# Kernel tuning notes

Hardware: AMD Instinct MI355X
Metric: run time of the kernel (lower is better)

The kernel has to match this reference:

```python
import jax, jax.numpy as jnp
import numpy as np

B, S, D = 2, 2048, 1024
H, DC = 16, 16          # num_heads, head_coord_dim
CD = 16                 # coord_dim
DH = D // H             # head_dim = 64


def setup_inputs() -> dict:
    key = jax.random.key(0)
    ks = jax.random.split(key, 8)
    s = 0.02
    return {
        "hidden_states": jax.random.normal(ks[0], (B, S, D), jnp.float32),
        "coordinates": jax.random.normal(ks[1], (B, S, CD), jnp.float32),
        "Wv": jax.random.normal(ks[2], (D, D), jnp.float32) * s,
        "bv": jnp.zeros((D,), jnp.float32),
        "Wc": jax.random.normal(ks[3], (H * DC, CD), jnp.float32) * s,
        "bc": jnp.zeros((H * DC,), jnp.float32),
        "Wn": jax.random.normal(ks[4], (CD, D), jnp.float32) * s,
        "bn": jnp.zeros((CD,), jnp.float32),
        "Wo": jax.random.normal(ks[5], (D, D), jnp.float32) * s,
        "bo": jnp.zeros((D,), jnp.float32),
        "gamma": jnp.zeros((1, H, 1, 1), jnp.float32),
    }


def reference(hidden_states, coordinates, Wv, bv, Wc, bc, Wn, bn, Wo, bo, gamma):
    # value: [B,S,D] -> [B,H,S,DH]
    value = (hidden_states @ Wv.T + bv).reshape(B, S, H, DH).transpose(0, 2, 1, 3)
    # coordinate heads: [B,S,CD] -> [B,H,S,DC]
    z = (coordinates @ Wc.T + bc).reshape(B, S, H, DC).transpose(0, 2, 1, 3)
    z_sq = jnp.sum(z * z, axis=-1, keepdims=True)           # [B,H,S,1]
    # pairwise squared distances [B,H,S,S]
    sq_dist = z_sq + jnp.swapaxes(z_sq, -1, -2) - 2.0 * jnp.einsum("bhsc,bhtc->bhst", z, z)
    sq_dist = jnp.maximum(sq_dist, 0.0)
    g = jax.nn.softplus(gamma)                               # [1,H,1,1]
    attn = jax.nn.softmax(-g * sq_dist, axis=-1)             # [B,H,S,S]
    out = jnp.einsum("bhst,bhtd->bhsd", attn, value)         # [B,H,S,DH]
    out = out.transpose(0, 2, 1, 3).reshape(B, S, D)
    updated_hidden = out @ Wo.T + bo
    updated_coords = hidden_states @ Wn.T + bn               # [B,S,CD]
    return updated_hidden, updated_coords
```

## Files before the change

kernel.cpp:

```cpp
#include <hip/hip_runtime.h>
#include <math.h>

typedef short short8 __attribute__((ext_vector_type(8)));
typedef short short4t __attribute__((ext_vector_type(4)));
typedef float f32x4  __attribute__((ext_vector_type(4)));

#define AS1 __attribute__((address_space(1)))
#define AS3 __attribute__((address_space(3)))

__device__ __forceinline__ unsigned cvt_pk_bf16(float lo, float hi) {
    unsigned r;
    asm("v_cvt_pk_bf16_f32 %0, %1, %2" : "=v"(r) : "v"(lo), "v"(hi));
    return r;
}
__device__ __forceinline__ unsigned f2bf_rne(float x) {
    unsigned u = __float_as_uint(x);
    return (u + 0x7fffu + ((u >> 16) & 1u)) >> 16;
}
__device__ __forceinline__ float exp2_fast(float x) {
    float r;
    asm("v_exp_f32 %0, %1" : "=v"(r) : "v"(x));
    return r;
}
__device__ __forceinline__ f32x4 mfma_k16(short4t a, short4t b, f32x4 c) {
#if __has_builtin(__builtin_amdgcn_mfma_f32_16x16x16bf16_1k)
    return __builtin_amdgcn_mfma_f32_16x16x16bf16_1k(a, b, c, 0, 0, 0);
#else
    asm volatile("v_mfma_f32_16x16x16_bf16 %0, %1, %2, %0" : "+v"(c) : "v"(a), "v"(b));
    return c;
#endif
}

__global__ __launch_bounds__(256) void f2bf_all(const float* __restrict__ hidden,
                                                const float* __restrict__ Wv,
                                                const float* __restrict__ Wo,
                                                const float* __restrict__ Wn,
                                                short* __restrict__ hsb,
                                                short* __restrict__ Wvb,
                                                short* __restrict__ Wob,
                                                short* __restrict__ Wnb) {
    const int i = blockIdx.x * 256 + threadIdx.x;
    const float* src;
    short* dst;
    int ii;
    if (i < 524288)      { src = hidden; dst = hsb; ii = i; }
    else if (i < 655360) { src = Wv; dst = Wvb; ii = i - 524288; }
    else if (i < 786432) { src = Wo; dst = Wob; ii = i - 655360; }
    else                 { src = Wn; dst = Wnb; ii = i - 786432; }
    const float4 a = ((const float4*)src)[2 * ii];
    const float4 b = ((const float4*)src)[2 * ii + 1];
    uint4 r;
    r.x = cvt_pk_bf16(a.x, a.y);
    r.y = cvt_pk_bf16(a.z, a.w);
    r.z = cvt_pk_bf16(b.x, b.y);
    r.w = cvt_pk_bf16(b.z, b.w);
    ((uint4*)dst)[ii] = r;
}

__global__ __launch_bounds__(256) void zker3(const float* __restrict__ coords,
                                             const float* __restrict__ Wc,
                                             const float* __restrict__ bc,
                                             const float* __restrict__ gamma,
                                             short* __restrict__ ZA,
                                             short* __restrict__ ZB) {
    const int bs = blockIdx.x;
    const int b = bs >> 11, s = bs & 2047;
    const int tid = threadIdx.x;
    __shared__ float csh[16];
    if (tid < 16) csh[tid] = coords[(size_t)bs * 16 + tid];
    __syncthreads();
    float z = bc[tid];
#pragma unroll
    for (int k = 0; k < 16; k++) z = fmaf(csh[k], Wc[tid * 16 + k], z);
    const unsigned ub = f2bf_rne(z);
    const float zb = __uint_as_float(ub << 16);
    float sq = zb * zb;
    sq += __shfl_xor(sq, 1, 64);
    sq += __shfl_xor(sq, 2, 64);
    sq += __shfl_xor(sq, 4, 64);
    sq += __shfl_xor(sq, 8, 64);
    const int h = tid >> 4, c = tid & 15;
    const float gm = gamma[h];
    const float sp = fmaxf(gm, 0.f) + log1pf(__expf(-fabsf(gm)));
    const float ch = -sp * 1.4426950408889634f;
    const size_t row = ((size_t)(b * 16 + h) * 2048 + s) * 32;
    ZA[row + c] = (short)ub;
    ZA[row + 16 + c] = (c == 0) ? (short)f2bf_rne(sq)
                                : (c == 1 ? (short)0x3F80 : (short)0);
    ZB[row + c] = (short)f2bf_rne(-2.f * ch * zb);
    ZB[row + 16 + c] = (c == 0) ? (short)f2bf_rne(ch)
                                : (c == 1 ? (short)f2bf_rne(ch * sq) : (short)0);
}

template <int EPI>
__global__ __launch_bounds__(256) void gemm_mfma(const short* __restrict__ A,
                                                 const short* __restrict__ W,
                                                 const float* __restrict__ bias,
                                                 void* __restrict__ Cout) {
    __shared__ short As[2][128][64];
    __shared__ short Bs[2][64][64];
    const int tid = threadIdx.x;
    const int wv = tid >> 6, l = tid & 63, g = l >> 4, qc = l & 15;
    const int wm = wv >> 1, wn = wv & 1;
    const int Mb = blockIdx.y * 128, Nb = blockIdx.x * 64;

    auto stage = [&](int buf, int k0) {
#pragma unroll
        for (int i = 0; i < 4; i++) {
            const int c = i * 256 + tid;
            const int r = c >> 3, jp = c & 7;
            const int js = jp ^ (r & 7);
            const short* gsA = A + (size_t)(Mb + r) * 1024 + k0 + js * 8;
            short* ldsA = &As[buf][0][0] + (size_t)(i * 256 + wv * 64) * 8;
            __builtin_amdgcn_global_load_lds((const AS1 void*)gsA, (AS3 void*)ldsA, 16, 0, 0);
        }
#pragma unroll
        for (int i = 0; i < 2; i++) {
            const int c = i * 256 + tid;
            const int r = c >> 3, jp = c & 7;
            const int js = jp ^ (r & 7);
            const short* gsB = W + (size_t)(Nb + r) * 1024 + k0 + js * 8;
            short* ldsB = &Bs[buf][0][0] + (size_t)(i * 256 + wv * 64) * 8;
            __builtin_amdgcn_global_load_lds((const AS1 void*)gsB, (AS3 void*)ldsB, 16, 0, 0);
        }
    };

    f32x4 acc[4][2] = {};
    stage(0, 0);
    __syncthreads();
    int cur = 0;
#pragma unroll 1
    for (int kb = 0; kb < 16; kb++) {
        if (kb < 15) stage(cur ^ 1, (kb + 1) * 64);
#pragma unroll
        for (int ks = 0; ks < 2; ks++) {
            const int cs = ((ks * 4 + g) ^ (qc & 7)) * 8;
            short8 af[4], bfr[2];
#pragma unroll
            for (int mt = 0; mt < 4; mt++)
                af[mt] = *(const short8*)&As[cur][wm * 64 + mt * 16 + qc][cs];
#pragma unroll
            for (int nt = 0; nt < 2; nt++)
                bfr[nt] = *(const short8*)&Bs[cur][wn * 32 + nt * 16 + qc][cs];
#pragma unroll
            for (int mt = 0; mt < 4; mt++)
#pragma unroll
                for (int nt = 0; nt < 2; nt++)
                    acc[mt][nt] = __builtin_amdgcn_mfma_f32_16x16x32_bf16(af[mt], bfr[nt], acc[mt][nt], 0, 0, 0);
        }
        __syncthreads();
        cur ^= 1;
    }

    float bl[2];
#pragma unroll
    for (int nt = 0; nt < 2; nt++) bl[nt] = bias[Nb + wn * 32 + nt * 16 + qc];
#pragma unroll
    for (int mt = 0; mt < 4; mt++) {
#pragma unroll
        for (int nt = 0; nt < 2; nt++) {
            const int m0 = Mb + wm * 64 + mt * 16 + g * 4;
            const int n  = Nb + wn * 32 + nt * 16 + qc;
            f32x4 v = acc[mt][nt];
            v = v + bl[nt];
            if (EPI == 0) {
                const int bb = m0 >> 11, s0 = m0 & 2047;
                const int hh = n >> 6, dh = n & 63;
                const int s0x = s0 ^ (((n >> 3) & 1) << 2);
                uint2 p2;
                p2.x = cvt_pk_bf16(v[0], v[1]);
                p2.y = cvt_pk_bf16(v[2], v[3]);
                *(uint2*)((short*)Cout + (size_t)((bb * 16 + hh) * 64 + dh) * 2048 + s0x) = p2;
            } else {
                float* C = (float*)Cout;
#pragma unroll
                for (int i = 0; i < 4; i++) C[(size_t)(m0 + i) * 1024 + n] = v[i];
            }
        }
    }
}

__global__ __launch_bounds__(256, 4) void attn_mfma10(const short* __restrict__ ZAg,
                                                      const short* __restrict__ ZBg,
                                                      const short* __restrict__ Vt,
                                                      short* __restrict__ AOb) {
    __shared__ short Vs[2][4096];
    __shared__ short Zs[3][2048];
    const int tid = threadIdx.x;
    const int wv = tid >> 6, ln = tid & 63, g = ln >> 4, qc = ln & 15;
    const int lin = blockIdx.x;
    const int work = (lin & 7) * 128 + (lin >> 3);
    const int qb = work & 31, h = (work >> 5) & 15, b = work >> 9;
    const int bh = b * 16 + h;
    const int q0 = qb * 64 + wv * 16;

    const short* ZAb = ZAg + (size_t)bh * (2048 * 32);
    const short* ZBb = ZBg + (size_t)bh * (2048 * 32);
    const short* Vb  = Vt  + (size_t)bh * (64 * 2048);

    const short8 zq = *(const short8*)(ZBb + (size_t)(q0 + qc) * 32 + g * 8);

    f32x4 acc[4] = {};
    float lsum = 0.f;

    const short* gvb = Vb + (size_t)ln * 2048 + wv * 8;
    short* lvd = &Vs[0][0] + (size_t)tid * 8;
    short* lzd = &Zs[0][0] + (size_t)tid * 8;
    const int z_kt = tid >> 6, z_g = (tid >> 4) & 3, z_r = tid & 15;

    auto stageV = [&](int buf, int kb) {
        const short* gv = gvb + kb;
        short* lvb = lvd + buf * 4096;
        __builtin_amdgcn_global_load_lds((const AS1 void*)gv, (AS3 void*)lvb, 16, 0, 0);
        __builtin_amdgcn_global_load_lds((const AS1 void*)(gv + 32), (AS3 void*)(lvb + 2048), 16, 0, 0);
    };
    auto stageZ = [&](int buf, int kb) {
        const short* gz = ZAb + (size_t)(kb + z_kt * 16 + z_r) * 32 + z_g * 8;
        __builtin_amdgcn_global_load_lds((const AS1 void*)gz, (AS3 void*)(lzd + buf * 2048), 16, 0, 0);
    };

    const int vrd = (((g >> 1) * 64 + qc) * 8) + (((g & 1) ^ ((qc >> 3) & 1)) << 2);
    const int zrd = g * 128 + qc * 8;

    auto computeP = [&](int zbuf, unsigned pko[4][2], bool doL) {
        const short* Zc = &Zs[0][0] + zbuf * 2048;
        short8 zk[4];
#pragma unroll
        for (int kt = 0; kt < 4; kt++)
            zk[kt] = *(const short8*)(Zc + zrd + kt * 512);
        const f32x4 z4 = {0.f, 0.f, 0.f, 0.f};
#pragma unroll
        for (int kt = 0; kt < 4; kt++) {
            const f32x4 S = __builtin_amdgcn_mfma_f32_16x16x32_bf16(zk[kt], zq, z4, 0, 0, 0);
            const float p0 = exp2_fast(fminf(S[0], 0.f));
            const float p1 = exp2_fast(fminf(S[1], 0.f));
            const float p2 = exp2_fast(fminf(S[2], 0.f));
            const float p3 = exp2_fast(fminf(S[3], 0.f));
            if (doL) lsum += (p0 + p1) + (p2 + p3);
            pko[kt][0] = cvt_pk_bf16(p0, p1);
            pko[kt][1] = cvt_pk_bf16(p2, p3);
        }
    };

    stageV(0, 0);
    stageZ(0, 0);
    stageZ(1, 64);
    __syncthreads();

    unsigned pk[4][2];
    computeP(0, pk, true);

    int cur = 0;
    int zn = 1;
#pragma unroll 1
    for (int i = 0; i < 32; i++) {
        const int kb = i * 64;
        int zs = zn + 1; if (zs == 3) zs = 0;
        if (i < 31) stageV(cur ^ 1, kb + 64);
        if (i < 30) stageZ(zs, kb + 128);

        unsigned pknext[4][2];
        computeP(zn, pknext, i < 31);

        const short* Vc = &Vs[cur][0];
        __builtin_amdgcn_s_setprio(1);
#pragma unroll
        for (int kt = 0; kt < 4; kt++) {
            union { unsigned u[2]; short4t s4; } pb;
            pb.u[0] = pk[kt][0];
            pb.u[1] = pk[kt][1];
#pragma unroll
            for (int mt = 0; mt < 4; mt++)
                acc[mt] = mfma_k16(*(const short4t*)(Vc + vrd + kt * 1024 + mt * 128),
                                   pb.s4, acc[mt]);
        }
        __builtin_amdgcn_s_setprio(0);

#pragma unroll
        for (int kt = 0; kt < 4; kt++) {
            pk[kt][0] = pknext[kt][0];
            pk[kt][1] = pknext[kt][1];
        }

        __syncthreads();
        cur ^= 1;
        zn = zs;
    }

    lsum += __shfl_xor(lsum, 16, 64);
    lsum += __shfl_xor(lsum, 32, 64);
    const float inv = 1.f / lsum;
    const size_t row = (size_t)(b * 2048 + q0 + qc) * 1024 + h * 64;
#pragma unroll
    for (int mt = 0; mt < 4; mt++) {
        uint2 o;
        o.x = cvt_pk_bf16(acc[mt][0] * inv, acc[mt][1] * inv);
        o.y = cvt_pk_bf16(acc[mt][2] * inv, acc[mt][3] * inv);
        *(uint2*)(AOb + row + mt * 16 + g * 4) = o;
    }
}

__global__ __launch_bounds__(256) void coords_mfma(const short* __restrict__ A,
                                                   const short* __restrict__ Wnb,
                                                   const float* __restrict__ bn,
                                                   float* __restrict__ out1) {
    __shared__ float red[4][16][16];
    const int tid = threadIdx.x;
    const int wv = tid >> 6, l = tid & 63, g = l >> 4, qc = l & 15;
    const int m0 = blockIdx.x * 16;
    const int k0 = wv * 256;
    f32x4 acc = {};
#pragma unroll
    for (int kk = 0; kk < 256; kk += 32) {
        const short8 af = *(const short8*)(A + (size_t)(m0 + qc) * 1024 + k0 + kk + g * 8);
        const short8 bf = *(const short8*)(Wnb + (size_t)qc * 1024 + k0 + kk + g * 8);
        acc = __builtin_amdgcn_mfma_f32_16x16x32_bf16(af, bf, acc, 0, 0, 0);
    }
#pragma unroll
    for (int i2 = 0; i2 < 4; i2++) red[wv][g * 4 + i2][qc] = acc[i2];
    __syncthreads();
    const int r = tid >> 4, c = tid & 15;
    const float s = red[0][r][c] + red[1][r][c] + red[2][r][c] + red[3][r][c] + bn[c];
    out1[(size_t)(m0 + r) * 16 + c] = s;
}

extern "C" void kernel_launch(void* const* d_in, const int* in_sizes, int n_in,
                              void* d_out, int out_size, void* d_ws, size_t ws_size,
                              hipStream_t stream) {
    (void)in_sizes; (void)n_in; (void)out_size; (void)ws_size;
    const float* hidden = (const float*)d_in[0];
    const float* coords = (const float*)d_in[1];
    const float* Wv = (const float*)d_in[2];
    const float* bv = (const float*)d_in[3];
    const float* Wc = (const float*)d_in[4];
    const float* bc = (const float*)d_in[5];
    const float* Wn = (const float*)d_in[6];
    const float* bn = (const float*)d_in[7];
    const float* Wo = (const float*)d_in[8];
    const float* bo = (const float*)d_in[9];
    const float* gamma = (const float*)d_in[10];

    char* wsb = (char*)d_ws;
    short* hsb = (short*)(wsb);
    short* AOb = hsb;
    short* Wvb = (short*)(wsb + (8 << 20));
    short* Wob = (short*)(wsb + (10 << 20));
    short* Vt  = (short*)(wsb + (12 << 20));
    short* ZA  = (short*)(wsb + (20 << 20));
    short* ZB  = (short*)(wsb + (24 << 20));
    short* Wnb = (short*)(wsb + (28 << 20));

    float* out_hidden = (float*)d_out;
    float* out_coords = out_hidden + 4194304;

    f2bf_all<<<3080, 256, 0, stream>>>(hidden, Wv, Wo, Wn, hsb, Wvb, Wob, Wnb);
    zker3<<<4096, 256, 0, stream>>>(coords, Wc, bc, gamma, ZA, ZB);
    gemm_mfma<0><<<dim3(16, 32), 256, 0, stream>>>(hsb, Wvb, bv, (void*)Vt);
    coords_mfma<<<256, 256, 0, stream>>>(hsb, Wnb, bn, out_coords);
    attn_mfma10<<<1024, 256, 0, stream>>>(ZA, ZB, Vt, AOb);
    gemm_mfma<1><<<dim3(16, 32), 256, 0, stream>>>(AOb, Wob, bo, (void*)out_hidden);
}
```

Measured before the change: 108.7 us.

## Drop LDS staging in attention; read V and Z directly into registers

The V projection epilogue now writes values in a fragment-friendly tiled layout (16 keys by 64 dims per chunk), so the attention kernel can load MFMA operands straight from global memory into registers. The LDS double/triple buffers and per-iteration __syncthreads are removed. Z keys are prefetched one iteration ahead in registers. The goal is to cut LDS traffic and barrier stalls, at the cost of losing cross-wave sharing of V tiles: each of the four waves now reads the same V chunk from L2/cache separately, and there is less latency hiding.

```diff
diff --git a/kernel.cpp b/kernel.cpp
--- a/kernel.cpp
+++ b/kernel.cpp
@@ -166,11 +166,11 @@
             if (EPI == 0) {
                 const int bb = m0 >> 11, s0 = m0 & 2047;
                 const int hh = n >> 6, dh = n & 63;
-                const int s0x = s0 ^ (((n >> 3) & 1) << 2);
+                const int kc = s0 >> 4, si = s0 & 15;
                 uint2 p2;
                 p2.x = cvt_pk_bf16(v[0], v[1]);
                 p2.y = cvt_pk_bf16(v[2], v[3]);
-                *(uint2*)((short*)Cout + (size_t)((bb * 16 + hh) * 64 + dh) * 2048 + s0x) = p2;
+                *(uint2*)((short*)Cout + (size_t)(bb * 16 + hh) * 131072 + kc * 1024 + dh * 16 + si) = p2;
             } else {
                 float* C = (float*)Cout;
 #pragma unroll
@@ -180,12 +180,10 @@
     }
 }
 
-__global__ __launch_bounds__(256, 4) void attn_mfma10(const short* __restrict__ ZAg,
+__global__ __launch_bounds__(256, 4) void attn_mfma11(const short* __restrict__ ZAg,
                                                       const short* __restrict__ ZBg,
                                                       const short* __restrict__ Vt,
                                                       short* __restrict__ AOb) {
-    __shared__ short Vs[2][4096];
-    __shared__ short Zs[3][2048];
     const int tid = threadIdx.x;
     const int wv = tid >> 6, ln = tid & 63, g = ln >> 4, qc = ln & 15;
     const int lin = blockIdx.x;
@@ -196,73 +194,60 @@
 
     const short* ZAb = ZAg + (size_t)bh * (2048 * 32);
     const short* ZBb = ZBg + (size_t)bh * (2048 * 32);
-    const short* Vb  = Vt  + (size_t)bh * (64 * 2048);
+    const short* Vb  = Vt  + (size_t)bh * 131072;
 
     const short8 zq = *(const short8*)(ZBb + (size_t)(q0 + qc) * 32 + g * 8);
 
     f32x4 acc[4] = {};
     float lsum = 0.f;
 
-    const short* gvb = Vb + (size_t)ln * 2048 + wv * 8;
-    short* lvd = &Vs[0][0] + (size_t)tid * 8;
-    short* lzd = &Zs[0][0] + (size_t)tid * 8;
-    const int z_kt = tid >> 6, z_g = (tid >> 4) & 3, z_r = tid & 15;
-
-    auto stageV = [&](int buf, int kb) {
-        const short* gv = gvb + kb;
-        short* lvb = lvd + buf * 4096;
-        __builtin_amdgcn_global_load_lds((const AS1 void*)gv, (AS3 void*)lvb, 16, 0, 0);
-        __builtin_amdgcn_global_load_lds((const AS1 void*)(gv + 32), (AS3 void*)(lvb + 2048), 16, 0, 0);
-    };
-    auto stageZ = [&](int buf, int kb) {
-        const short* gz = ZAb + (size_t)(kb + z_kt * 16 + z_r) * 32 + z_g * 8;
-        __builtin_amdgcn_global_load_lds((const AS1 void*)gz, (AS3 void*)(lzd + buf * 2048), 16, 0, 0);
-    };
-
-    const int vrd = (((g >> 1) * 64 + qc) * 8) + (((g & 1) ^ ((qc >> 3) & 1)) << 2);
-    const int zrd = g * 128 + qc * 8;
-
-    auto computeP = [&](int zbuf, unsigned pko[4][2], bool doL) {
-        const short* Zc = &Zs[0][0] + zbuf * 2048;
-        short8 zk[4];
-#pragma unroll
-        for (int kt = 0; kt < 4; kt++)
-            zk[kt] = *(const short8*)(Zc + zrd + kt * 512);
-        const f32x4 z4 = {0.f, 0.f, 0.f, 0.f};
-#pragma unroll
-        for (int kt = 0; kt < 4; kt++) {
-            const f32x4 S = __builtin_amdgcn_mfma_f32_16x16x32_bf16(zk[kt], zq, z4, 0, 0, 0);
-            const float p0 = exp2_fast(fminf(S[0], 0.f));
-            const float p1 = exp2_fast(fminf(S[1], 0.f));
-            const float p2 = exp2_fast(fminf(S[2], 0.f));
-            const float p3 = exp2_fast(fminf(S[3], 0.f));
-            if (doL) lsum += (p0 + p1) + (p2 + p3);
-            pko[kt][0] = cvt_pk_bf16(p0, p1);
-            pko[kt][1] = cvt_pk_bf16(p2, p3);
-        }
-    };
-
-    stageV(0, 0);
-    stageZ(0, 0);
-    stageZ(1, 64);
-    __syncthreads();
-
-    unsigned pk[4][2];
-    computeP(0, pk, true);
-
-    int cur = 0;
-    int zn = 1;
+    const short* zbase = ZAb + (size_t)qc * 32 + g * 8;
+    const short* vbase = Vb + qc * 16 + g * 4;
+
+    short8 zkc[4];
+#pragma unroll
+    for (int kt = 0; kt < 4; kt++)
+        zkc[kt] = *(const short8*)(zbase + (size_t)(kt * 16) * 32);
+
 #pragma unroll 1
     for (int i = 0; i < 32; i++) {
         const int kb = i * 64;
-        int zs = zn + 1; if (zs == 3) zs = 0;
-        if (i < 31) stageV(cur ^ 1, kb + 64);
-        if (i < 30) stageZ(zs, kb + 128);
-
-        unsigned pknext[4][2];
-        computeP(zn, pknext, i < 31);
-
-        const short* Vc = &Vs[cur][0];
+
+        short8 zkn[4];
+        if (i < 31) {
+#pragma unroll
+            for (int kt = 0; kt < 4; kt++)
+                zkn[kt] = *(const short8*)(zbase + (size_t)(kb + 64 + kt * 16) * 32);
+        }
+
+        short4t vf[4][4];
+        const short* vk = vbase + (size_t)(i * 4) * 1024;
+#pragma unroll
+        for (int kt = 0; kt < 4; kt++)
+#pragma unroll
+            for (int mt = 0; mt < 4; mt++)
+                vf[kt][mt] = *(const short4t*)(vk + kt * 1024 + mt * 256);
+
+        const f32x4 z4 = {0.f, 0.f, 0.f, 0.f};
+        f32x4 S[4];
+        __builtin_amdgcn_s_setprio(1);
+#pragma unroll
+        for (int kt = 0; kt < 4; kt++)
+            S[kt] = __builtin_amdgcn_mfma_f32_16x16x32_bf16(zkc[kt], zq, z4, 0, 0, 0);
+        __builtin_amdgcn_s_setprio(0);
+
+        unsigned pk[4][2];
+#pragma unroll
+        for (int kt = 0; kt < 4; kt++) {
+            const float p0 = exp2_fast(fminf(S[kt][0], 0.f));
+            const float p1 = exp2_fast(fminf(S[kt][1], 0.f));
+            const float p2 = exp2_fast(fminf(S[kt][2], 0.f));
+            const float p3 = exp2_fast(fminf(S[kt][3], 0.f));
+            lsum += (p0 + p1) + (p2 + p3);
+            pk[kt][0] = cvt_pk_bf16(p0, p1);
+            pk[kt][1] = cvt_pk_bf16(p2, p3);
+        }
+
         __builtin_amdgcn_s_setprio(1);
 #pragma unroll
         for (int kt = 0; kt < 4; kt++) {
@@ -271,20 +256,14 @@
             pb.u[1] = pk[kt][1];
 #pragma unroll
             for (int mt = 0; mt < 4; mt++)
-                acc[mt] = mfma_k16(*(const short4t*)(Vc + vrd + kt * 1024 + mt * 128),
-                                   pb.s4, acc[mt]);
+                acc[mt] = mfma_k16(vf[kt][mt], pb.s4, acc[mt]);
         }
         __builtin_amdgcn_s_setprio(0);
 
-#pragma unroll
-        for (int kt = 0; kt < 4; kt++) {
-            pk[kt][0] = pknext[kt][0];
-            pk[kt][1] = pknext[kt][1];
-        }
-
-        __syncthreads();
-        cur ^= 1;
-        zn = zs;
+        if (i < 31) {
+#pragma unroll
+            for (int kt = 0; kt < 4; kt++) zkc[kt] = zkn[kt];
+        }
     }
 
     lsum += __shfl_xor(lsum, 16, 64);
@@ -357,6 +336,6 @@
     zker3<<<4096, 256, 0, stream>>>(coords, Wc, bc, gamma, ZA, ZB);
     gemm_mfma<0><<<dim3(16, 32), 256, 0, stream>>>(hsb, Wvb, bv, (void*)Vt);
     coords_mfma<<<256, 256, 0, stream>>>(hsb, Wnb, bn, out_coords);
-    attn_mfma10<<<1024, 256, 0, stream>>>(ZA, ZB, Vt, AOb);
+    attn_mfma11<<<1024, 256, 0, stream>>>(ZA, ZB, Vt, AOb);
     gemm_mfma<1><<<dim3(16, 32), 256, 0, stream>>>(AOb, Wob, bo, (void*)out_hidden);
 }
```

After: 147.8 us. 35.9% more time.

## Compute softmax row sums via MFMA, unroll attention loop by two, remap GEMM blocks

Applied to the files above, without the earlier changes.

The attention kernel drops the per-element scalar row-sum accumulation and instead gets the softmax denominator from an extra MFMA against a ones vector. It also unrolls the main loop by two with ping-pong P registers and a four-deep Z buffer, which removes the register copy and the modular buffer arithmetic. The GEMM launches switch to a 1D grid remapped so that consecutive blocks land on different XCDs with grouped M tiles, aiming for better L2 reuse. The trade-offs are more LDS for Z, one extra MFMA per k-tile, and a row sum taken from bf16-rounded P values.

```diff
diff --git a/kernel.cpp b/kernel.cpp
--- a/kernel.cpp
+++ b/kernel.cpp
@@ -102,7 +102,9 @@
     const int tid = threadIdx.x;
     const int wv = tid >> 6, l = tid & 63, g = l >> 4, qc = l & 15;
     const int wm = wv >> 1, wn = wv & 1;
-    const int Mb = blockIdx.y * 128, Nb = blockIdx.x * 64;
+    const int lin = blockIdx.x;
+    const int wid = (lin & 7) * 64 + (lin >> 3);
+    const int Mb = (wid & 31) * 128, Nb = (wid >> 5) * 64;
 
     auto stage = [&](int buf, int k0) {
 #pragma unroll
@@ -180,12 +182,12 @@
     }
 }
 
-__global__ __launch_bounds__(256, 4) void attn_mfma10(const short* __restrict__ ZAg,
+__global__ __launch_bounds__(256, 4) void attn_mfma12(const short* __restrict__ ZAg,
                                                       const short* __restrict__ ZBg,
                                                       const short* __restrict__ Vt,
                                                       short* __restrict__ AOb) {
     __shared__ short Vs[2][4096];
-    __shared__ short Zs[3][2048];
+    __shared__ short Zs[4][2048];
     const int tid = threadIdx.x;
     const int wv = tid >> 6, ln = tid & 63, g = ln >> 4, qc = ln & 15;
     const int lin = blockIdx.x;
@@ -200,8 +202,11 @@
 
     const short8 zq = *(const short8*)(ZBb + (size_t)(q0 + qc) * 32 + g * 8);
 
+    union { unsigned u[2]; short4t s4; } ones4;
+    ones4.u[0] = ones4.u[1] = (qc == 0) ? 0x3F803F80u : 0u;
+
     f32x4 acc[4] = {};
-    float lsum = 0.f;
+    f32x4 accl = {};
 
     const short* gvb = Vb + (size_t)ln * 2048 + wv * 8;
     short* lvd = &Vs[0][0] + (size_t)tid * 8;
@@ -222,7 +227,7 @@
     const int vrd = (((g >> 1) * 64 + qc) * 8) + (((g & 1) ^ ((qc >> 3) & 1)) << 2);
     const int zrd = g * 128 + qc * 8;
 
-    auto computeP = [&](int zbuf, unsigned pko[4][2], bool doL) {
+    auto computeP = [&](int zbuf, unsigned pko[4][2]) {
         const short* Zc = &Zs[0][0] + zbuf * 2048;
         short8 zk[4];
 #pragma unroll
@@ -232,14 +237,25 @@
 #pragma unroll
         for (int kt = 0; kt < 4; kt++) {
             const f32x4 S = __builtin_amdgcn_mfma_f32_16x16x32_bf16(zk[kt], zq, z4, 0, 0, 0);
-            const float p0 = exp2_fast(fminf(S[0], 0.f));
-            const float p1 = exp2_fast(fminf(S[1], 0.f));
-            const float p2 = exp2_fast(fminf(S[2], 0.f));
-            const float p3 = exp2_fast(fminf(S[3], 0.f));
-            if (doL) lsum += (p0 + p1) + (p2 + p3);
-            pko[kt][0] = cvt_pk_bf16(p0, p1);
-            pko[kt][1] = cvt_pk_bf16(p2, p3);
-        }
+            pko[kt][0] = cvt_pk_bf16(exp2_fast(fminf(S[0], 0.f)), exp2_fast(fminf(S[1], 0.f)));
+            pko[kt][1] = cvt_pk_bf16(exp2_fast(fminf(S[2], 0.f)), exp2_fast(fminf(S[3], 0.f)));
+        }
+    };
+    auto doPV = [&](int buf, unsigned pkk[4][2]) {
+        const short* Vc = &Vs[buf][0];
+        __builtin_amdgcn_s_setprio(1);
+#pragma unroll
+        for (int kt = 0; kt < 4; kt++) {
+            union { unsigned u[2]; short4t s4; } pb;
+            pb.u[0] = pkk[kt][0];
+            pb.u[1] = pkk[kt][1];
+            accl = mfma_k16(ones4.s4, pb.s4, accl);
+#pragma unroll
+            for (int mt = 0; mt < 4; mt++)
+                acc[mt] = mfma_k16(*(const short4t*)(Vc + vrd + kt * 1024 + mt * 128),
+                                   pb.s4, acc[mt]);
+        }
+        __builtin_amdgcn_s_setprio(0);
     };
 
     stageV(0, 0);
@@ -247,49 +263,28 @@
     stageZ(1, 64);
     __syncthreads();
 
-    unsigned pk[4][2];
-    computeP(0, pk, true);
+    unsigned pkA[4][2], pkB[4][2];
+    computeP(0, pkA);
 
     int cur = 0;
-    int zn = 1;
 #pragma unroll 1
-    for (int i = 0; i < 32; i++) {
-        const int kb = i * 64;
-        int zs = zn + 1; if (zs == 3) zs = 0;
-        if (i < 31) stageV(cur ^ 1, kb + 64);
-        if (i < 30) stageZ(zs, kb + 128);
-
-        unsigned pknext[4][2];
-        computeP(zn, pknext, i < 31);
-
-        const short* Vc = &Vs[cur][0];
-        __builtin_amdgcn_s_setprio(1);
-#pragma unroll
-        for (int kt = 0; kt < 4; kt++) {
-            union { unsigned u[2]; short4t s4; } pb;
-            pb.u[0] = pk[kt][0];
-            pb.u[1] = pk[kt][1];
-#pragma unroll
-            for (int mt = 0; mt < 4; mt++)
-                acc[mt] = mfma_k16(*(const short4t*)(Vc + vrd + kt * 1024 + mt * 128),
-                                   pb.s4, acc[mt]);
-        }
-        __builtin_amdgcn_s_setprio(0);
-
-#pragma unroll
-        for (int kt = 0; kt < 4; kt++) {
-            pk[kt][0] = pknext[kt][0];
-            pk[kt][1] = pknext[kt][1];
-        }
-
+    for (int i = 0; i < 32; i += 2) {
+        if (i < 31) stageV(cur ^ 1, (i + 1) * 64);
+        if (i < 30) stageZ((i + 2) & 3, (i + 2) * 64);
+        computeP((i + 1) & 3, pkB);
+        doPV(cur, pkA);
         __syncthreads();
         cur ^= 1;
-        zn = zs;
-    }
-
-    lsum += __shfl_xor(lsum, 16, 64);
-    lsum += __shfl_xor(lsum, 32, 64);
-    const float inv = 1.f / lsum;
+        if (i + 1 < 31) stageV(cur ^ 1, (i + 2) * 64);
+        if (i + 1 < 30) stageZ((i + 3) & 3, (i + 3) * 64);
+        computeP((i + 2) & 3, pkA);
+        doPV(cur, pkB);
+        __syncthreads();
+        cur ^= 1;
+    }
+
+    const float lv2 = __shfl(accl[0], qc, 64);
+    const float inv = 1.f / lv2;
     const size_t row = (size_t)(b * 2048 + q0 + qc) * 1024 + h * 64;
 #pragma unroll
     for (int mt = 0; mt < 4; mt++) {
@@ -355,8 +350,8 @@
 
     f2bf_all<<<3080, 256, 0, stream>>>(hidden, Wv, Wo, Wn, hsb, Wvb, Wob, Wnb);
     zker3<<<4096, 256, 0, stream>>>(coords, Wc, bc, gamma, ZA, ZB);
-    gemm_mfma<0><<<dim3(16, 32), 256, 0, stream>>>(hsb, Wvb, bv, (void*)Vt);
+    gemm_mfma<0><<<512, 256, 0, stream>>>(hsb, Wvb, bv, (void*)Vt);
     coords_mfma<<<256, 256, 0, stream>>>(hsb, Wnb, bn, out_coords);
-    attn_mfma10<<<1024, 256, 0, stream>>>(ZA, ZB, Vt, AOb);
-    gemm_mfma<1><<<dim3(16, 32), 256, 0, stream>>>(AOb, Wob, bo, (void*)out_hidden);
-}
+    attn_mfma12<<<1024, 256, 0, stream>>>(ZA, ZB, Vt, AOb);
+    gemm_mfma<1><<<512, 256, 0, stream>>>(AOb, Wob, bo, (void*)out_hidden);
+}
```

Result: no change. 106.9 us (-1.7%).
